# Performance work log

Measured on AMD Instinct MI355X. Metric: run time of the kernel, lower is better.

Reference implementation:

```python
import jax, jax.numpy as jnp
import numpy as np

M, N, D = 16384, 128, 2048  # actions, question tokens, ExpSet.dim


def setup_inputs() -> dict:
    key = jax.random.key(0)
    ks = jax.random.split(key, 6)
    s1 = 1.0 / np.sqrt(2 * D)  # torch Linear default init bounds
    s2 = 1.0 / np.sqrt(D)
    return {
        "action_embedding": jax.random.normal(ks[0], (M, D), jnp.float32),
        "question_t": jax.random.normal(ks[1], (N, D), jnp.float32),
        "history_t": jax.random.normal(ks[2], (D,), jnp.float32),
        "W1": jax.random.uniform(ks[3], (D, 2 * D), jnp.float32, -s1, s1),
        "b1": jnp.zeros((D,), jnp.float32),
        "W2": jax.random.uniform(ks[4], (D, D), jnp.float32, -s2, s2),
        "b2": jnp.zeros((D,), jnp.float32),
    }


def reference(action_embedding, question_t, history_t, W1, b1, W2, b2):
    # Attention: each action (query) attends over the n question tokens.
    # Equivalent to expand->attend->sum in the torch code, but without
    # materializing the [m, n, d] expanded tensor.
    scores = action_embedding @ question_t.T              # [M, N]
    attn = jax.nn.softmax(scores, axis=1)                 # softmax over tokens
    question = attn @ question_t                          # [M, D] (attended + summed)

    # Perceptron(2d -> d -> d) on cat([history, question])
    hist = jnp.broadcast_to(history_t, (action_embedding.shape[0], history_t.shape[0]))
    qh = jnp.concatenate([hist, question], axis=1)        # [M, 2D]
    h = jax.nn.relu(qh @ W1.T + b1)                       # [M, D]
    qwh = h @ W2.T + b2                                   # [M, D]

    # Elementwise dot with action embeddings, softmax over actions.
    semantic_scores = jnp.sum(qwh * action_embedding, axis=1)  # [M]
    return jax.nn.softmax(semantic_scores, axis=0)
```

## Files before the change

kernel.cpp:

```cpp
#include <hip/hip_runtime.h>
#include <hip/hip_bf16.h>


typedef _Float16 f16;
typedef __attribute__((ext_vector_type(8))) _Float16 half8;
typedef __attribute__((ext_vector_type(4))) _Float16 half4_t;
typedef __attribute__((ext_vector_type(4))) float f32x4;

#define GLL(gp, lp)                                                              \
  __builtin_amdgcn_global_load_lds(                                              \
      (const __attribute__((address_space(1))) void*)(gp),                       \
      (__attribute__((address_space(3))) void*)(lp), 16, 0, 0)

#define WAITN(n)                                                                 \
  do {                                                                           \
    asm volatile("s_waitcnt vmcnt(" #n ")" ::: "memory");                        \
    __builtin_amdgcn_sched_barrier(0);                                           \
  } while (0)

#define MFMA16(a, b, c) __builtin_amdgcn_mfma_f32_16x16x32_f16(a, b, c, 0, 0, 0)

template <int NT, int LDA, int LDB>
__device__ __forceinline__ void kloop1(const f16* __restrict__ A,
                                       const f16* __restrict__ B,
                                       f16* __restrict__ SM,
                                       f32x4 (&acc)[4][4],
                                       int lane, int wv, int wm, int wn) {
  static_assert(NT >= 4, "depth-3 pipeline needs NT >= 4");
  const int f = lane & 15, kk = lane >> 4;
  const int cS = (lane & 7) ^ (lane >> 3);
  const int kkS = (cS & 3) * 8;
  const int rS = 2 * (lane >> 3) + (cS >> 2);
  const size_t offA0 = (size_t)(16 * (wv * 2 + 0) + rS) * LDA + kkS;
  const size_t offA1 = (size_t)(16 * (wv * 2 + 1) + rS) * LDA + kkS;
  const size_t offB0 = (size_t)(16 * (wv * 2 + 0) + rS) * LDB + kkS;
  const size_t offB1 = (size_t)(16 * (wv * 2 + 1) + rS) * LDB + kkS;
  const int Ld0 = (wv * 2 + 0) * 512, Ld1 = (wv * 2 + 1) * 512;

  int aoff[4], boff[4];
  #pragma unroll
  for (int mf = 0; mf < 4; ++mf) {
    const int R = wm + mf * 16 + f;
    const int c2 = (((R & 1) << 2) | kk) ^ ((R >> 1) & 7);
    aoff[mf] = (R >> 1) * 64 + c2 * 8;
  }
  #pragma unroll
  for (int nf = 0; nf < 4; ++nf) {
    const int R = wn + nf * 16 + f;
    const int c2 = (((R & 1) << 2) | kk) ^ ((R >> 1) & 7);
    boff[nf] = (R >> 1) * 64 + c2 * 8;
  }

  auto STAGE = [&](int set, int kt) {
    f16* base = SM + set * 8192;
    GLL(A + offA0 + kt, base + Ld0);
    GLL(A + offA1 + kt, base + Ld1);
    GLL(B + offB0 + kt, base + 4096 + Ld0);
    GLL(B + offB1 + kt, base + 4096 + Ld1);
  };
  auto COMPUTE = [&](int set) {
    const f16* p = SM + set * 8192;
    half8 a[4], b[4];
    #pragma unroll
    for (int mf = 0; mf < 4; ++mf) a[mf] = *(const half8*)&p[aoff[mf]];
    #pragma unroll
    for (int nf = 0; nf < 4; ++nf) b[nf] = *(const half8*)&p[4096 + boff[nf]];
    __builtin_amdgcn_s_setprio(1);
    #pragma unroll
    for (int mf = 0; mf < 4; ++mf)
      #pragma unroll
      for (int nf = 0; nf < 4; ++nf)
        acc[mf][nf] = MFMA16(a[mf], b[nf], acc[mf][nf]);
    __builtin_amdgcn_s_setprio(0);
  };

  STAGE(0, 0);
  STAGE(1, 32);
  STAGE(2, 64);
  #pragma unroll 1
  for (int t = 0; t < NT - 3; ++t) {
    STAGE((t + 3) & 3, (t + 3) * 32);
    WAITN(12);
    __builtin_amdgcn_s_barrier();
    COMPUTE(t & 3);
    __builtin_amdgcn_s_barrier();
  }
  WAITN(8);
  __builtin_amdgcn_s_barrier();
  COMPUTE((NT - 3) & 3);
  __builtin_amdgcn_s_barrier();
  WAITN(4);
  __builtin_amdgcn_s_barrier();
  COMPUTE((NT - 2) & 3);
  __builtin_amdgcn_s_barrier();
  WAITN(0);
  __builtin_amdgcn_s_barrier();
  COMPUTE((NT - 1) & 3);
  __builtin_amdgcn_s_barrier();
}

template <int NT, int LDA, int LDB>
__device__ __forceinline__ void kloop256(const f16* __restrict__ A,
                                         const f16* __restrict__ B,
                                         f16* __restrict__ SM,
                                         f32x4 (&acc)[8][4],
                                         int lane, int wv, int wm, int wn) {
  static_assert(NT >= 3, "pipeline needs NT >= 3");
  const int f = lane & 15, kk = lane >> 4;
  const int cS = (lane & 7) ^ (lane >> 3);
  const int kkS = (cS & 3) * 8;
  const int rS = 2 * (lane >> 3) + (cS >> 2);
  const size_t offA0 = (size_t)(16 * (wv * 2 + 0) + rS) * LDA + kkS;
  const size_t offA1 = (size_t)(16 * (wv * 2 + 1) + rS) * LDA + kkS;
  const size_t offB0 = (size_t)(16 * (wv * 2 + 0) + rS) * LDB + kkS;
  const size_t offB1 = (size_t)(16 * (wv * 2 + 1) + rS) * LDB + kkS;
  const int Ld0 = (wv * 2 + 0) * 512, Ld1 = (wv * 2 + 1) * 512;

  int aoff[8], boff[4];
  #pragma unroll
  for (int mf = 0; mf < 8; ++mf) {
    const int R = wm + mf * 16 + f;
    const int c2 = (((R & 1) << 2) | kk) ^ ((R >> 1) & 7);
    aoff[mf] = (R >> 1) * 64 + c2 * 8;
  }
  #pragma unroll
  for (int nf = 0; nf < 4; ++nf) {
    const int R = wn + nf * 16 + f;
    const int c2 = (((R & 1) << 2) | kk) ^ ((R >> 1) & 7);
    boff[nf] = 8192 + (R >> 1) * 64 + c2 * 8;
  }

  auto STAGE = [&](int set, int kt) {
    f16* base = SM + set * 16384;
    GLL(A + offA0 + kt, base + Ld0);
    GLL(A + offA1 + kt, base + Ld1);
    GLL(B + offB0 + kt, base + 8192 + Ld0);
    GLL(B + offB1 + kt, base + 8192 + Ld1);
  };
  auto COMPUTE = [&](int set) {
    const f16* p = SM + set * 16384;
    half8 a[8], b[4];
    #pragma unroll
    for (int mf = 0; mf < 8; ++mf) a[mf] = *(const half8*)&p[aoff[mf]];
    #pragma unroll
    for (int nf = 0; nf < 4; ++nf) b[nf] = *(const half8*)&p[boff[nf]];
    __builtin_amdgcn_s_setprio(1);
    #pragma unroll
    for (int mf = 0; mf < 8; ++mf)
      #pragma unroll
      for (int nf = 0; nf < 4; ++nf)
        acc[mf][nf] = MFMA16(a[mf], b[nf], acc[mf][nf]);
    __builtin_amdgcn_s_setprio(0);
  };

  STAGE(0, 0);
  STAGE(1, 32);
  #pragma unroll 1
  for (int t = 0; t < NT - 2; ++t) {
    STAGE((t + 2) & 3, (t + 2) * 32);
    WAITN(8);
    __builtin_amdgcn_s_barrier();
    COMPUTE(t & 3);
  }
  WAITN(4);
  __builtin_amdgcn_s_barrier();
  COMPUTE((NT - 2) & 3);
  WAITN(0);
  __builtin_amdgcn_s_barrier();
  COMPUTE((NT - 1) & 3);
}


__global__ __launch_bounds__(256) void c_kernel(const float* __restrict__ W1,
                                                const float* __restrict__ b1,
                                                const float* __restrict__ hist,
                                                float* __restrict__ c) {
  const int wave = threadIdx.x >> 6, lane = threadIdx.x & 63;
  const int j = blockIdx.x * 4 + wave;
  const float* row = W1 + (size_t)j * 4096;
  float s = 0.f;
  #pragma unroll 2
  for (int kq = lane; kq < 512; kq += 64) {
    const float4 w = *(const float4*)&row[kq * 4];
    const float4 h = *(const float4*)&hist[kq * 4];
    s += w.x * h.x + w.y * h.y + w.z * h.z + w.w * h.w;
  }
  #pragma unroll
  for (int mask = 1; mask < 64; mask <<= 1) s += __shfl_xor(s, mask);
  if (lane == 0) c[j] = s + b1[j];
}

__device__ __forceinline__ half4_t f16hi4(const float4 v) {
  half4_t h;
  h.x = (f16)v.x; h.y = (f16)v.y; h.z = (f16)v.z; h.w = (f16)v.w;
  return h;
}

__global__ __launch_bounds__(256) void prep_AQ(const float* __restrict__ A,
                                               const float* __restrict__ Q,
                                               const float* __restrict__ b2,
                                               f16* __restrict__ Af,
                                               f16* __restrict__ Qf,
                                               float* __restrict__ ab2) {
  const int wv = threadIdx.x >> 6, lane = threadIdx.x & 63;
  if (blockIdx.x < 4096) {
    const size_t row = (size_t)blockIdx.x * 4 + wv;
    const float* ar = A + row * 2048;
    float dot = 0.f;
    #pragma unroll 2
    for (int c0 = 0; c0 < 2048; c0 += 256) {
      const int col = c0 + lane * 4;
      const float4 v = *(const float4*)&ar[col];
      const float4 bb = *(const float4*)&b2[col];
      dot += v.x * bb.x + v.y * bb.y + v.z * bb.z + v.w * bb.w;
      *(half4_t*)&Af[row * 2048 + col] = f16hi4(v);
    }
    #pragma unroll
    for (int mask = 1; mask < 64; mask <<= 1) dot += __shfl_xor(dot, mask);
    if (lane == 0) ab2[row] = dot;
  } else {
    const size_t row = (size_t)(blockIdx.x - 4096) * 4 + wv;
    const float* qr = Q + row * 2048;
    #pragma unroll 2
    for (int c0 = 0; c0 < 2048; c0 += 256) {
      const int col = c0 + lane * 4;
      const float4 v = *(const float4*)&qr[col];
      *(half4_t*)&Qf[row * 2048 + col] = f16hi4(v);
    }
  }
}

__global__ __launch_bounds__(256) void transpose_f16(const float* __restrict__ src,
                                                     int R, int C,
                                                     f16* __restrict__ dst) {
  __shared__ float T[64][65];
  const int c0 = blockIdx.x * 64, r0 = blockIdx.y * 64;
  const int t = threadIdx.x;
  {
    const int rl = t >> 4, cl = (t & 15) * 4;
    #pragma unroll
    for (int ii = 0; ii < 4; ++ii) {
      const float4 v = *(const float4*)&src[(size_t)(r0 + rl + ii * 16) * C + c0 + cl];
      T[rl + ii * 16][cl + 0] = v.x; T[rl + ii * 16][cl + 1] = v.y;
      T[rl + ii * 16][cl + 2] = v.z; T[rl + ii * 16][cl + 3] = v.w;
    }
  }
  __syncthreads();
  const int cc = t >> 2, rr0 = (t & 3) * 16;
  f16 u[16];
  #pragma unroll
  for (int k = 0; k < 16; ++k) u[k] = (f16)T[rr0 + k][cc];
  f16* ph = dst + (size_t)(c0 + cc) * R + r0 + rr0;
  #pragma unroll
  for (int k4 = 0; k4 < 4; ++k4)
    *(half4_t*)&ph[k4 * 4] = *(half4_t*)&u[k4 * 4];
}

template <int BM, int TM>
__global__ __launch_bounds__(256) void gemm_bt_sk(const float* __restrict__ A,
                                                  const float* __restrict__ B,
                                                  float* __restrict__ Cpart,
                                                  int Kslab, int lda, int ldb,
                                                  int ldc, int M) {
  constexpr int BN = 64, BK = 32;
  constexpr int ASTR = BM + 12, BSTR = BN + 4;
  __shared__ float As[BK][ASTR];
  __shared__ float Bs[BK][BSTR];
  const int tid = threadIdx.x;
  const int tx = tid & 15, ty = tid >> 4;
  const int m0 = ty * TM, n0 = tx * 4;
  const size_t bm = (size_t)blockIdx.x * BM, bn = (size_t)blockIdx.y * BN;
  const int kb = blockIdx.z * Kslab;
  const float* Ab = A + bm * lda;
  const float* Bb = B + bn * ldb;
  float acc[TM][4];
  #pragma unroll
  for (int i = 0; i < TM; ++i)
    #pragma unroll
    for (int j = 0; j < 4; ++j) acc[i][j] = 0.f;
  for (int kt = kb; kt < kb + Kslab; kt += BK) {
    #pragma unroll
    for (int it = 0; it < BM * BK / 4 / 256; ++it) {
      const int idx = it * 256 + tid;
      const int row = idx >> 3, kq = idx & 7;
      const float4 v = *(const float4*)&Ab[(size_t)row * lda + kt + kq * 4];
      As[kq * 4 + 0][row] = v.x; As[kq * 4 + 1][row] = v.y;
      As[kq * 4 + 2][row] = v.z; As[kq * 4 + 3][row] = v.w;
    }
    #pragma unroll
    for (int it = 0; it < BN * BK / 4 / 256; ++it) {
      const int idx = it * 256 + tid;
      const int row = idx >> 3, kq = idx & 7;
      const float4 v = *(const float4*)&Bb[(size_t)row * ldb + kt + kq * 4];
      Bs[kq * 4 + 0][row] = v.x; Bs[kq * 4 + 1][row] = v.y;
      Bs[kq * 4 + 2][row] = v.z; Bs[kq * 4 + 3][row] = v.w;
    }
    __syncthreads();
    #pragma unroll
    for (int k = 0; k < BK; ++k) {
      float av[TM];
      #pragma unroll
      for (int i = 0; i < TM; ++i) av[i] = As[k][m0 + i];
      const float4 b = *(const float4*)&Bs[k][n0];
      const float bv[4] = {b.x, b.y, b.z, b.w};
      #pragma unroll
      for (int i = 0; i < TM; ++i)
        #pragma unroll
        for (int j = 0; j < 4; ++j) acc[i][j] = fmaf(av[i], bv[j], acc[i][j]);
    }
    __syncthreads();
  }
  float* base = Cpart + (size_t)blockIdx.z * M * ldc;
  #pragma unroll
  for (int i = 0; i < TM; ++i) {
    float* crow = base + (bm + m0 + i) * (size_t)ldc + bn + n0;
    #pragma unroll
    for (int j = 0; j < 4; ++j) crow[j] = acc[i][j];
  }
}

__global__ __launch_bounds__(256) void qwt_combine(const float* __restrict__ part,
                                                   f16* __restrict__ QWt) {
  const size_t i = ((size_t)blockIdx.x * 256 + threadIdx.x) * 4;
  float4 s = make_float4(0.f, 0.f, 0.f, 0.f);
  #pragma unroll
  for (int z = 0; z < 8; ++z) {
    const float4 v = *(const float4*)&part[(size_t)z * 262144 + i];
    s.x += v.x; s.y += v.y; s.z += v.z; s.w += v.w;
  }
  *(half4_t*)&QWt[i] = f16hi4(s);
}

__global__ __launch_bounds__(256, 2) void s_attn_sk(const f16* __restrict__ Af,
                                                    const f16* __restrict__ Qf,
                                                    float* __restrict__ Sp) {
  __shared__ f16 SM[32768];
  const int tid = threadIdx.x, lane = tid & 63, wv = tid >> 6;
  const int wm = (wv >> 1) * 64, wn = (wv & 1) * 64;
  const int f = lane & 15, kk = lane >> 4;
  const size_t bm = (size_t)(blockIdx.x >> 1) * 128;
  const int kz = blockIdx.x & 1;

  f32x4 acc[4][4];
  #pragma unroll
  for (int mf = 0; mf < 4; ++mf)
    #pragma unroll
    for (int nf = 0; nf < 4; ++nf) acc[mf][nf] = 0.f;

  kloop1<32, 2048, 2048>(Af + bm * 2048 + kz * 1024, Qf + kz * 1024,
                         SM, acc, lane, wv, wm, wn);

  float* out = Sp + (size_t)kz * 16384 * 128;
  #pragma unroll
  for (int mf = 0; mf < 4; ++mf)
    #pragma unroll
    for (int r = 0; r < 4; ++r) {
      const size_t row = bm + wm + mf * 16 + kk * 4 + r;
      #pragma unroll
      for (int nf = 0; nf < 4; ++nf)
        out[row * 128 + wn + nf * 16 + f] = acc[mf][nf][r];
    }
}

__global__ __launch_bounds__(256) void softmax_at(const float* __restrict__ Sp,
                                                  f16* __restrict__ at) {
  const int tid = threadIdx.x;
  const int sub = tid & 7;
  const size_t row = (size_t)blockIdx.x * 32 + (tid >> 3);
  const float* p0 = Sp + row * 128 + sub * 16;
  const float* p1 = p0 + (size_t)16384 * 128;
  float v[16];
  #pragma unroll
  for (int q = 0; q < 4; ++q) {
    const float4 a = ((const float4*)p0)[q];
    const float4 b = ((const float4*)p1)[q];
    v[q * 4 + 0] = a.x + b.x; v[q * 4 + 1] = a.y + b.y;
    v[q * 4 + 2] = a.z + b.z; v[q * 4 + 3] = a.w + b.w;
  }
  float mx = v[0];
  #pragma unroll
  for (int e = 1; e < 16; ++e) mx = fmaxf(mx, v[e]);
  mx = fmaxf(mx, __shfl_xor(mx, 1));
  mx = fmaxf(mx, __shfl_xor(mx, 2));
  mx = fmaxf(mx, __shfl_xor(mx, 4));
  float sm = 0.f;
  #pragma unroll
  for (int e = 0; e < 16; ++e) { v[e] = __expf(v[e] - mx); sm += v[e]; }
  sm += __shfl_xor(sm, 1);
  sm += __shfl_xor(sm, 2);
  sm += __shfl_xor(sm, 4);
  const float inv = 1.0f / sm;
  f16* po = at + row * 128 + sub * 16;
  #pragma unroll
  for (int q = 0; q < 4; ++q) {
    half4_t h;
    h.x = (f16)(v[q * 4 + 0] * inv); h.y = (f16)(v[q * 4 + 1] * inv);
    h.z = (f16)(v[q * 4 + 2] * inv); h.w = (f16)(v[q * 4 + 3] * inv);
    *(half4_t*)&po[q * 4] = h;
  }
}

__global__ __launch_bounds__(256, 2) void h_kernel(const f16* __restrict__ at,
                                                   const f16* __restrict__ QWt,
                                                   const float* __restrict__ cvec,
                                                   f16* __restrict__ H) {
  __shared__ f16 SM[32768];
  const int tid = threadIdx.x, lane = tid & 63, wv = tid >> 6;
  const int wm = (wv >> 1) * 64, wn = (wv & 1) * 64;
  const int f = lane & 15, kk = lane >> 4;
  const size_t bm = (size_t)(blockIdx.x & 127) * 128;
  const size_t bn = (size_t)(blockIdx.x >> 7) * 128;

  f32x4 acc[4][4];
  #pragma unroll
  for (int mf = 0; mf < 4; ++mf)
    #pragma unroll
    for (int nf = 0; nf < 4; ++nf) acc[mf][nf] = 0.f;

  kloop1<4, 128, 128>(at + bm * 128, QWt + bn * 128, SM, acc, lane, wv, wm, wn);

  float ccv[4];
  #pragma unroll
  for (int nf = 0; nf < 4; ++nf) ccv[nf] = cvec[bn + wn + nf * 16 + f];

  __syncthreads();
  constexpr int STR = 136;
  f16* T = SM;
  #pragma unroll
  for (int mf = 0; mf < 4; ++mf)
    #pragma unroll
    for (int r = 0; r < 4; ++r) {
      const int row = wm + mf * 16 + kk * 4 + r;
      #pragma unroll
      for (int nf = 0; nf < 4; ++nf)
        T[row * STR + wn + nf * 16 + f] =
            (f16)fmaxf(acc[mf][nf][r] + ccv[nf], 0.f);
    }
  __syncthreads();
  #pragma unroll
  for (int it = 0; it < 8; ++it) {
    const int row = it * 16 + (tid >> 4);
    const int ch = tid & 15;
    const float4 vv = *(const float4*)&T[row * STR + ch * 8];
    *(float4*)&H[(bm + row) * 2048 + bn + ch * 8] = vv;
  }
}

__global__ __launch_bounds__(512, 1) void fused_g(
    const f16* __restrict__ Af, const f16* __restrict__ H,
    const f16* __restrict__ W2t, float* __restrict__ partial) {
  extern __shared__ f16 SM[];
  const int tid = threadIdx.x, lane = tid & 63, wv = tid >> 6;
  const int wm = (wv >> 2) * 128, wn = (wv & 3) * 64;
  const int f = lane & 15, kk = lane >> 4;
  const int lin = blockIdx.x;
  const int sid = (lin & 7) * 64 + (lin >> 3);
  const int bmI = sid & 63, bnI = sid >> 6;
  const size_t bm = (size_t)bmI * 256;
  const size_t bn = (size_t)bnI * 256;

  f32x4 acc[8][4];
  #pragma unroll
  for (int mf = 0; mf < 8; ++mf)
    #pragma unroll
    for (int nf = 0; nf < 4; ++nf) acc[mf][nf] = 0.f;

  kloop256<64, 2048, 2048>(Af + bm * 2048, W2t + bn * 2048, SM, acc, lane, wv, wm, wn);

  float part[8][4];
  #pragma unroll
  for (int mf = 0; mf < 8; ++mf)
    #pragma unroll
    for (int r = 0; r < 4; ++r) {
      const size_t hrow = (bm + wm + mf * 16 + kk * 4 + r) * 2048 + bn + wn + f;
      float s = 0.f;
      #pragma unroll
      for (int nf = 0; nf < 4; ++nf)
        s += (float)H[hrow + nf * 16] * acc[mf][nf][r];
      part[mf][r] = s;
    }
  #pragma unroll
  for (int mf = 0; mf < 8; ++mf)
    #pragma unroll
    for (int r = 0; r < 4; ++r) {
      part[mf][r] += __shfl_xor(part[mf][r], 1);
      part[mf][r] += __shfl_xor(part[mf][r], 2);
      part[mf][r] += __shfl_xor(part[mf][r], 4);
      part[mf][r] += __shfl_xor(part[mf][r], 8);
    }
  if (f == 0) {
    const size_t slab = (size_t)(bnI * 4 + (wv & 3)) * 16384;
    #pragma unroll
    for (int mf = 0; mf < 8; ++mf)
      #pragma unroll
      for (int r = 0; r < 4; ++r)
        partial[slab + bm + wm + mf * 16 + kk * 4 + r] = part[mf][r];
  }
}


__global__ __launch_bounds__(256) void k_sem(const float* __restrict__ partial,
                                             const float* __restrict__ ab2,
                                             float* __restrict__ semantic,
                                             float* __restrict__ bstats) {
  const int m = blockIdx.x * 256 + threadIdx.x;
  float s = ab2[m];
  #pragma unroll
  for (int nb = 0; nb < 32; ++nb) s += partial[(size_t)nb * 16384 + m];
  semantic[m] = s;
  float mx = s;
  #pragma unroll
  for (int mask = 1; mask < 64; mask <<= 1) mx = fmaxf(mx, __shfl_xor(mx, mask));
  __shared__ float wmax[4], wsum[4];
  const int wave = threadIdx.x >> 6, lane = threadIdx.x & 63;
  if (lane == 0) wmax[wave] = mx;
  __syncthreads();
  const float bmax = fmaxf(fmaxf(wmax[0], wmax[1]), fmaxf(wmax[2], wmax[3]));
  float e = expf(s - bmax);
  #pragma unroll
  for (int mask = 1; mask < 64; mask <<= 1) e += __shfl_xor(e, mask);
  if (lane == 0) wsum[wave] = e;
  __syncthreads();
  if (threadIdx.x == 0) {
    bstats[blockIdx.x * 2] = bmax;
    bstats[blockIdx.x * 2 + 1] = wsum[0] + wsum[1] + wsum[2] + wsum[3];
  }
}

__global__ __launch_bounds__(256) void k_out(const float* __restrict__ semantic,
                                             const float* __restrict__ bstats,
                                             float* __restrict__ out) {
  __shared__ float g0s, g1s;
  const int tid = threadIdx.x;
  if (tid < 64) {
    const float bm = bstats[tid * 2], bs = bstats[tid * 2 + 1];
    float gm = bm;
    #pragma unroll
    for (int mask = 1; mask < 64; mask <<= 1) gm = fmaxf(gm, __shfl_xor(gm, mask));
    float gs = bs * expf(bm - gm);
    #pragma unroll
    for (int mask = 1; mask < 64; mask <<= 1) gs += __shfl_xor(gs, mask);
    if (tid == 0) { g0s = gm; g1s = gs; }
  }
  __syncthreads();
  const int m = blockIdx.x * 256 + tid;
  out[m] = expf(semantic[m] - g0s) / g1s;
}


extern "C" void kernel_launch(void* const* d_in, const int* in_sizes, int n_in,
                              void* d_out, int out_size, void* d_ws, size_t ws_size,
                              hipStream_t stream) {
  (void)in_sizes; (void)n_in; (void)out_size; (void)ws_size;
  const float* A    = (const float*)d_in[0];
  const float* Q    = (const float*)d_in[1];
  const float* hist = (const float*)d_in[2];
  const float* W1   = (const float*)d_in[3];
  const float* b1   = (const float*)d_in[4];
  const float* W2   = (const float*)d_in[5];
  const float* b2   = (const float*)d_in[6];
  float* out = (float*)d_out;

  char* ws = (char*)d_ws;
  f16* Af      = (f16*)ws;   ws += (size_t)16384 * 2048 * 2;
  f16* Hbuf    = (f16*)ws;   ws += (size_t)16384 * 2048 * 2;
  f16* W2t     = (f16*)ws;   ws += (size_t)2048 * 2048 * 2;
  f16* Qf      = (f16*)ws;   ws += (size_t)128 * 2048 * 2;
  f16* QWt     = (f16*)ws;   ws += (size_t)2048 * 128 * 2;
  f16* at      = (f16*)ws;   ws += (size_t)16384 * 128 * 2;
  float* qwt_part = (float*)ws; ws += (size_t)8 * 2048 * 128 * 4;
  float* Sp    = (float*)ws; ws += (size_t)2 * 16384 * 128 * 4;
  float* c_vec = (float*)ws; ws += 2048 * 4;
  float* ab2   = (float*)ws; ws += 16384 * 4;
  float* partial  = (float*)ws; ws += (size_t)32 * 16384 * 4;
  float* semantic = (float*)ws; ws += 16384 * 4;
  float* bstats   = (float*)ws; ws += 128 * 4;

  hipFuncSetAttribute((const void*)fused_g,
                      hipFuncAttributeMaxDynamicSharedMemorySize, 131072);

  c_kernel<<<512, 256, 0, stream>>>(W1, b1, hist, c_vec);
  gemm_bt_sk<32, 2><<<dim3(64, 2, 8), 256, 0, stream>>>(W1 + 2048, Q, qwt_part,
                                                        256, 4096, 2048, 128, 2048);
  qwt_combine<<<256, 256, 0, stream>>>(qwt_part, QWt);
  transpose_f16<<<dim3(32, 32), 256, 0, stream>>>(W2, 2048, 2048, W2t);
  prep_AQ<<<4128, 256, 0, stream>>>(A, Q, b2, Af, Qf, ab2);
  s_attn_sk<<<256, 256, 0, stream>>>(Af, Qf, Sp);
  softmax_at<<<512, 256, 0, stream>>>(Sp, at);
  h_kernel<<<2048, 256, 0, stream>>>(at, QWt, c_vec, Hbuf);
  fused_g<<<512, 512, 131072, stream>>>(Af, Hbuf, W2t, partial);
  k_sem<<<64, 256, 0, stream>>>(partial, ab2, semantic, bstats);
  k_out<<<64, 256, 0, stream>>>(semantic, bstats, out);
}
```

Before: 269.7 us.

## Pre-pack W2 in MFMA fragment layout and load B directly into registers

W2 is now transposed into a fragment-packed layout so each wave can load its B operands straight from global memory into registers, double-buffered across k-steps. Only the A tile is staged through LDS, which halves shared memory per block to 64KB and allows two blocks per CU. The wave tiling changes from 128x64 to 64x128, which halves the number of partial-sum slabs that k_sem reduces. The cost is that B fragments are fetched per wave from global/L2 with no LDS sharing, adding register pressure and repeated global traffic.

```diff
diff --git a/kernel.cpp b/kernel.cpp
--- a/kernel.cpp
+++ b/kernel.cpp
@@ -97,77 +97,6 @@
   __builtin_amdgcn_s_barrier();
   COMPUTE((NT - 1) & 3);
   __builtin_amdgcn_s_barrier();
-}
-
-template <int NT, int LDA, int LDB>
-__device__ __forceinline__ void kloop256(const f16* __restrict__ A,
-                                         const f16* __restrict__ B,
-                                         f16* __restrict__ SM,
-                                         f32x4 (&acc)[8][4],
-                                         int lane, int wv, int wm, int wn) {
-  static_assert(NT >= 3, "pipeline needs NT >= 3");
-  const int f = lane & 15, kk = lane >> 4;
-  const int cS = (lane & 7) ^ (lane >> 3);
-  const int kkS = (cS & 3) * 8;
-  const int rS = 2 * (lane >> 3) + (cS >> 2);
-  const size_t offA0 = (size_t)(16 * (wv * 2 + 0) + rS) * LDA + kkS;
-  const size_t offA1 = (size_t)(16 * (wv * 2 + 1) + rS) * LDA + kkS;
-  const size_t offB0 = (size_t)(16 * (wv * 2 + 0) + rS) * LDB + kkS;
-  const size_t offB1 = (size_t)(16 * (wv * 2 + 1) + rS) * LDB + kkS;
-  const int Ld0 = (wv * 2 + 0) * 512, Ld1 = (wv * 2 + 1) * 512;
-
-  int aoff[8], boff[4];
-  #pragma unroll
-  for (int mf = 0; mf < 8; ++mf) {
-    const int R = wm + mf * 16 + f;
-    const int c2 = (((R & 1) << 2) | kk) ^ ((R >> 1) & 7);
-    aoff[mf] = (R >> 1) * 64 + c2 * 8;
-  }
-  #pragma unroll
-  for (int nf = 0; nf < 4; ++nf) {
-    const int R = wn + nf * 16 + f;
-    const int c2 = (((R & 1) << 2) | kk) ^ ((R >> 1) & 7);
-    boff[nf] = 8192 + (R >> 1) * 64 + c2 * 8;
-  }
-
-  auto STAGE = [&](int set, int kt) {
-    f16* base = SM + set * 16384;
-    GLL(A + offA0 + kt, base + Ld0);
-    GLL(A + offA1 + kt, base + Ld1);
-    GLL(B + offB0 + kt, base + 8192 + Ld0);
-    GLL(B + offB1 + kt, base + 8192 + Ld1);
-  };
-  auto COMPUTE = [&](int set) {
-    const f16* p = SM + set * 16384;
-    half8 a[8], b[4];
-    #pragma unroll
-    for (int mf = 0; mf < 8; ++mf) a[mf] = *(const half8*)&p[aoff[mf]];
-    #pragma unroll
-    for (int nf = 0; nf < 4; ++nf) b[nf] = *(const half8*)&p[boff[nf]];
-    __builtin_amdgcn_s_setprio(1);
-    #pragma unroll
-    for (int mf = 0; mf < 8; ++mf)
-      #pragma unroll
-      for (int nf = 0; nf < 4; ++nf)
-        acc[mf][nf] = MFMA16(a[mf], b[nf], acc[mf][nf]);
-    __builtin_amdgcn_s_setprio(0);
-  };
-
-  STAGE(0, 0);
-  STAGE(1, 32);
-  #pragma unroll 1
-  for (int t = 0; t < NT - 2; ++t) {
-    STAGE((t + 2) & 3, (t + 2) * 32);
-    WAITN(8);
-    __builtin_amdgcn_s_barrier();
-    COMPUTE(t & 3);
-  }
-  WAITN(4);
-  __builtin_amdgcn_s_barrier();
-  COMPUTE((NT - 2) & 3);
-  WAITN(0);
-  __builtin_amdgcn_s_barrier();
-  COMPUTE((NT - 1) & 3);
 }
 
 
@@ -230,9 +159,8 @@
   }
 }
 
-__global__ __launch_bounds__(256) void transpose_f16(const float* __restrict__ src,
-                                                     int R, int C,
-                                                     f16* __restrict__ dst) {
+__global__ __launch_bounds__(256) void transpose_pack(const float* __restrict__ src,
+                                                      f16* __restrict__ W2p) {
   __shared__ float T[64][65];
   const int c0 = blockIdx.x * 64, r0 = blockIdx.y * 64;
   const int t = threadIdx.x;
@@ -240,7 +168,7 @@
     const int rl = t >> 4, cl = (t & 15) * 4;
     #pragma unroll
     for (int ii = 0; ii < 4; ++ii) {
-      const float4 v = *(const float4*)&src[(size_t)(r0 + rl + ii * 16) * C + c0 + cl];
+      const float4 v = *(const float4*)&src[(size_t)(r0 + rl + ii * 16) * 2048 + c0 + cl];
       T[rl + ii * 16][cl + 0] = v.x; T[rl + ii * 16][cl + 1] = v.y;
       T[rl + ii * 16][cl + 2] = v.z; T[rl + ii * 16][cl + 3] = v.w;
     }
@@ -250,10 +178,16 @@
   f16 u[16];
   #pragma unroll
   for (int k = 0; k < 16; ++k) u[k] = (f16)T[rr0 + k][cc];
-  f16* ph = dst + (size_t)(c0 + cc) * R + r0 + rr0;
-  #pragma unroll
-  for (int k4 = 0; k4 < 4; ++k4)
-    *(half4_t*)&ph[k4 * 4] = *(half4_t*)&u[k4 * 4];
+  const int j = c0 + cc;
+  const int k0 = r0 + rr0;
+  const int rb = j >> 4, f = j & 15;
+  const int kb = k0 >> 5, kk0 = (k0 & 31) >> 3;
+  f16* p0 = W2p + ((size_t)(rb * 64 + kb) * 64 + kk0 * 16 + f) * 8;
+  f16* p1 = W2p + ((size_t)(rb * 64 + kb) * 64 + (kk0 + 1) * 16 + f) * 8;
+  *(half4_t*)&p0[0] = *(half4_t*)&u[0];
+  *(half4_t*)&p0[4] = *(half4_t*)&u[4];
+  *(half4_t*)&p1[0] = *(half4_t*)&u[8];
+  *(half4_t*)&p1[4] = *(half4_t*)&u[12];
 }
 
 template <int BM, int TM>
@@ -446,56 +380,124 @@
   }
 }
 
-__global__ __launch_bounds__(512, 1) void fused_g(
+__global__ __launch_bounds__(512, 2) void fused_g(
     const f16* __restrict__ Af, const f16* __restrict__ H,
-    const f16* __restrict__ W2t, float* __restrict__ partial) {
+    const f16* __restrict__ W2p, float* __restrict__ partial) {
   extern __shared__ f16 SM[];
   const int tid = threadIdx.x, lane = tid & 63, wv = tid >> 6;
-  const int wm = (wv >> 2) * 128, wn = (wv & 3) * 64;
+  const int wm = (wv >> 1) * 64;
+  const int wn = (wv & 1) * 128;
   const int f = lane & 15, kk = lane >> 4;
   const int lin = blockIdx.x;
   const int sid = (lin & 7) * 64 + (lin >> 3);
   const int bmI = sid & 63, bnI = sid >> 6;
   const size_t bm = (size_t)bmI * 256;
   const size_t bn = (size_t)bnI * 256;
-
-  f32x4 acc[8][4];
-  #pragma unroll
-  for (int mf = 0; mf < 8; ++mf)
-    #pragma unroll
-    for (int nf = 0; nf < 4; ++nf) acc[mf][nf] = 0.f;
-
-  kloop256<64, 2048, 2048>(Af + bm * 2048, W2t + bn * 2048, SM, acc, lane, wv, wm, wn);
-
-  float part[8][4];
-  #pragma unroll
-  for (int mf = 0; mf < 8; ++mf)
+  const f16* A = Af + bm * 2048;
+  const int rbase = (int)(bn >> 4) + (wn >> 4);
+
+  const int cS = (lane & 7) ^ (lane >> 3);
+  const int kkS = (cS & 3) * 8;
+  const int rS = 2 * (lane >> 3) + (cS >> 2);
+  const size_t offA0 = (size_t)(16 * (wv * 2 + 0) + rS) * 2048 + kkS;
+  const size_t offA1 = (size_t)(16 * (wv * 2 + 1) + rS) * 2048 + kkS;
+  const int Ld0 = (wv * 2 + 0) * 512, Ld1 = (wv * 2 + 1) * 512;
+
+  int aoff[4];
+  #pragma unroll
+  for (int mf = 0; mf < 4; ++mf) {
+    const int R = wm + mf * 16 + f;
+    const int c2 = (((R & 1) << 2) | kk) ^ ((R >> 1) & 7);
+    aoff[mf] = (R >> 1) * 64 + c2 * 8;
+  }
+
+  f32x4 acc[4][8];
+  #pragma unroll
+  for (int mf = 0; mf < 4; ++mf)
+    #pragma unroll
+    for (int nf = 0; nf < 8; ++nf) acc[mf][nf] = 0.f;
+
+  half8 bA[8], bB[8];
+
+#define STAGE_A(set, kt)                                                         \
+  do {                                                                           \
+    f16* base_ = SM + (set) * 8192;                                              \
+    GLL(A + offA0 + (kt), base_ + Ld0);                                          \
+    GLL(A + offA1 + (kt), base_ + Ld1);                                          \
+  } while (0)
+
+#define BLOAD(dst, t)                                                            \
+  do {                                                                           \
+    _Pragma("unroll")                                                            \
+    for (int nf = 0; nf < 8; ++nf)                                               \
+      dst[nf] = *(const half8*)&W2p[((size_t)(rbase + nf) * 64 + (t)) * 512 +    \
+                                    lane * 8];                                   \
+  } while (0)
+
+#define COMPUTE(set, b)                                                          \
+  do {                                                                           \
+    const f16* p_ = SM + (set) * 8192;                                           \
+    half8 a_[4];                                                                 \
+    _Pragma("unroll")                                                            \
+    for (int mf = 0; mf < 4; ++mf) a_[mf] = *(const half8*)&p_[aoff[mf]];        \
+    __builtin_amdgcn_s_setprio(1);                                               \
+    _Pragma("unroll")                                                            \
+    for (int mf = 0; mf < 4; ++mf)                                               \
+      _Pragma("unroll")                                                          \
+      for (int nf = 0; nf < 8; ++nf)                                             \
+        acc[mf][nf] = MFMA16(a_[mf], b[nf], acc[mf][nf]);                        \
+    __builtin_amdgcn_s_setprio(0);                                               \
+  } while (0)
+
+  BLOAD(bA, 0);
+  STAGE_A(0, 0);
+  STAGE_A(1, 32);
+  #pragma unroll 1
+  for (int t = 0; t < 62; t += 2) {
+    BLOAD(bB, t + 1);
+    STAGE_A((t + 2) & 3, (t + 2) * 32);
+    WAITN(10);
+    __builtin_amdgcn_s_barrier();
+    COMPUTE(t & 3, bA);
+    BLOAD(bA, t + 2);
+    STAGE_A((t + 3) & 3, (t + 3) * 32);
+    WAITN(10);
+    __builtin_amdgcn_s_barrier();
+    COMPUTE((t + 1) & 3, bB);
+  }
+  BLOAD(bB, 63);
+  WAITN(8);
+  __builtin_amdgcn_s_barrier();
+  COMPUTE(2, bA);
+  WAITN(0);
+  __builtin_amdgcn_s_barrier();
+  COMPUTE(3, bB);
+
+#undef STAGE_A
+#undef BLOAD
+#undef COMPUTE
+
+  float part[4][8];
+  #pragma unroll
+  for (int mf = 0; mf < 4; ++mf)
     #pragma unroll
     for (int r = 0; r < 4; ++r) {
       const size_t hrow = (bm + wm + mf * 16 + kk * 4 + r) * 2048 + bn + wn + f;
       float s = 0.f;
       #pragma unroll
-      for (int nf = 0; nf < 4; ++nf)
+      for (int nf = 0; nf < 8; ++nf)
         s += (float)H[hrow + nf * 16] * acc[mf][nf][r];
-      part[mf][r] = s;
-    }
-  #pragma unroll
-  for (int mf = 0; mf < 8; ++mf)
-    #pragma unroll
-    for (int r = 0; r < 4; ++r) {
-      part[mf][r] += __shfl_xor(part[mf][r], 1);
-      part[mf][r] += __shfl_xor(part[mf][r], 2);
-      part[mf][r] += __shfl_xor(part[mf][r], 4);
-      part[mf][r] += __shfl_xor(part[mf][r], 8);
-    }
-  if (f == 0) {
-    const size_t slab = (size_t)(bnI * 4 + (wv & 3)) * 16384;
-    #pragma unroll
-    for (int mf = 0; mf < 8; ++mf)
-      #pragma unroll
-      for (int r = 0; r < 4; ++r)
-        partial[slab + bm + wm + mf * 16 + kk * 4 + r] = part[mf][r];
-  }
+      s += __shfl_xor(s, 1);
+      s += __shfl_xor(s, 2);
+      s += __shfl_xor(s, 4);
+      s += __shfl_xor(s, 8);
+      part[mf][r & 3] = s;
+      if (f == 0) {
+        const size_t slab = (size_t)(bnI * 2 + (wv & 1)) * 16384;
+        partial[slab + bm + wm + mf * 16 + kk * 4 + r] = s;
+      }
+    }
+  (void)part;
 }
 
 
@@ -506,7 +508,7 @@
   const int m = blockIdx.x * 256 + threadIdx.x;
   float s = ab2[m];
   #pragma unroll
-  for (int nb = 0; nb < 32; ++nb) s += partial[(size_t)nb * 16384 + m];
+  for (int nb = 0; nb < 16; ++nb) s += partial[(size_t)nb * 16384 + m];
   semantic[m] = s;
   float mx = s;
   #pragma unroll
@@ -564,7 +566,7 @@
   char* ws = (char*)d_ws;
   f16* Af      = (f16*)ws;   ws += (size_t)16384 * 2048 * 2;
   f16* Hbuf    = (f16*)ws;   ws += (size_t)16384 * 2048 * 2;
-  f16* W2t     = (f16*)ws;   ws += (size_t)2048 * 2048 * 2;
+  f16* W2p     = (f16*)ws;   ws += (size_t)2048 * 2048 * 2;
   f16* Qf      = (f16*)ws;   ws += (size_t)128 * 2048 * 2;
   f16* QWt     = (f16*)ws;   ws += (size_t)2048 * 128 * 2;
   f16* at      = (f16*)ws;   ws += (size_t)16384 * 128 * 2;
@@ -572,23 +574,23 @@
   float* Sp    = (float*)ws; ws += (size_t)2 * 16384 * 128 * 4;
   float* c_vec = (float*)ws; ws += 2048 * 4;
   float* ab2   = (float*)ws; ws += 16384 * 4;
-  float* partial  = (float*)ws; ws += (size_t)32 * 16384 * 4;
+  float* partial  = (float*)ws; ws += (size_t)16 * 16384 * 4;
   float* semantic = (float*)ws; ws += 16384 * 4;
   float* bstats   = (float*)ws; ws += 128 * 4;
 
   hipFuncSetAttribute((const void*)fused_g,
-                      hipFuncAttributeMaxDynamicSharedMemorySize, 131072);
+                      hipFuncAttributeMaxDynamicSharedMemorySize, 65536);
 
   c_kernel<<<512, 256, 0, stream>>>(W1, b1, hist, c_vec);
   gemm_bt_sk<32, 2><<<dim3(64, 2, 8), 256, 0, stream>>>(W1 + 2048, Q, qwt_part,
                                                         256, 4096, 2048, 128, 2048);
   qwt_combine<<<256, 256, 0, stream>>>(qwt_part, QWt);
-  transpose_f16<<<dim3(32, 32), 256, 0, stream>>>(W2, 2048, 2048, W2t);
+  transpose_pack<<<dim3(32, 32), 256, 0, stream>>>(W2, W2p);
   prep_AQ<<<4128, 256, 0, stream>>>(A, Q, b2, Af, Qf, ab2);
   s_attn_sk<<<256, 256, 0, stream>>>(Af, Qf, Sp);
   softmax_at<<<512, 256, 0, stream>>>(Sp, at);
   h_kernel<<<2048, 256, 0, stream>>>(at, QWt, c_vec, Hbuf);
-  fused_g<<<512, 512, 131072, stream>>>(Af, Hbuf, W2t, partial);
+  fused_g<<<512, 512, 65536, stream>>>(Af, Hbuf, W2p, partial);
   k_sem<<<64, 256, 0, stream>>>(partial, ab2, semantic, bstats);
   k_out<<<64, 256, 0, stream>>>(semantic, bstats, out);
 }
```

New measurement: 288.6 us. 1.07x slower.
